# Kernel optimization log

Hardware: AMD Instinct MI355X
Metric: run time of the kernel (lower is better)

The kernel has to match this reference:

```python
import jax, jax.numpy as jnp
import numpy as np

BATCH = 4096
IN_SIZES = [1024, 1024, 1024, 1024]
EMB = 2048  # embracement_size


def setup_inputs() -> dict:
    key = jax.random.key(0)
    keys = jax.random.split(key, 3 * len(IN_SIZES))
    inp = {}
    for i, d in enumerate(IN_SIZES):
        inp[f"x{i}"] = jax.random.normal(keys[3 * i], (BATCH, d), dtype=jnp.float32)
        # Linear params (Kaiming-ish scale)
        inp[f"W{i}"] = jax.random.normal(keys[3 * i + 1], (d, EMB), dtype=jnp.float32) / np.sqrt(d)
        inp[f"b{i}"] = jax.random.normal(keys[3 * i + 2], (EMB,), dtype=jnp.float32) * 0.01
    return inp


def _sample_indices(batch, num_feats, emb):
    # availabilities=None, selection_probabilities=None -> uniform p over modalities
    # multinomial(p, num_samples=emb, replacement=True) == categorical over log p
    logits = jnp.zeros((batch, num_feats), dtype=jnp.float32)  # uniform
    k = jax.random.key(42)
    # shape (emb, batch) broadcasts against logits batch shape (batch,)
    idx = jax.random.categorical(k, logits, axis=-1, shape=(emb, batch))
    return idx.T  # [batch, emb]


def reference(x0, W0, b0, x1, W1, b1, x2, W2, b2, x3, W3, b3):
    xs = [x0, x1, x2, x3]
    Ws = [W0, W1, W2, W3]
    bs = [b0, b1, b2, b3]
    # docking: Linear + ReLU per modality -> [batch, EMB, num_feats]
    dock = jnp.stack([jax.nn.relu(x @ W + b) for x, W, b in zip(xs, Ws, bs)], axis=-1)
    B, E, F = dock.shape
    idx = _sample_indices(B, F, E)  # [B, E] int32
    # gather along modality axis (replaces one-hot multiply-sum)
    out = jnp.take_along_axis(dock, idx[:, :, None], axis=-1)[..., 0]
    return out  # [batch, EMB]
```

## Files before the change

### kernel.cpp

```cpp
#include <hip/hip_runtime.h>
#include <stdint.h>


typedef short short8 __attribute__((ext_vector_type(8)));
typedef float floatx4 __attribute__((ext_vector_type(4)));

#define B_DIM 4096
#define K_DIM 1024
#define E_DIM 2048

__device__ __forceinline__ uint32_t rotl32(uint32_t x, uint32_t r) {
  return __builtin_amdgcn_alignbit(x, x, 32u - r);
}

__device__ __forceinline__ uint16_t f2bf(float x) {
  uint32_t u = __float_as_uint(x);
  u += 0x7FFFu + ((u >> 16) & 1u);
  return (uint16_t)(u >> 16);
}

__device__ __forceinline__ void threefry(uint32_t x0, uint32_t x1,
                                         uint32_t& o0, uint32_t& o1) {
  const uint32_t ks0 = 0u;
  const uint32_t ks1 = 42u;
  const uint32_t ks2 = 0x1BD11BDAu ^ 42u;
  x0 += ks0; x1 += ks1;
#define TF_R(r) { x0 += x1; x1 = rotl32(x1, r); x1 ^= x0; }
  TF_R(13) TF_R(15) TF_R(26) TF_R(6)
  x0 += ks1; x1 += ks2 + 1u;
  TF_R(17) TF_R(29) TF_R(16) TF_R(24)
  x0 += ks2; x1 += ks0 + 2u;
  TF_R(13) TF_R(15) TF_R(26) TF_R(6)
  x0 += ks0; x1 += ks1 + 3u;
  TF_R(17) TF_R(29) TF_R(16) TF_R(24)
  x0 += ks1; x1 += ks2 + 4u;
  TF_R(13) TF_R(15) TF_R(26) TF_R(6)
  x0 += ks2; x1 += ks0 + 5u;
#undef TF_R
  o0 = x0; o1 = x1;
}

__global__ __launch_bounds__(256) void prep_kernel(
    const float* __restrict__ x0, const float* __restrict__ x1,
    const float* __restrict__ x2, const float* __restrict__ x3,
    const float* __restrict__ W0, const float* __restrict__ W1,
    const float* __restrict__ W2, const float* __restrict__ W3,
    uint16_t* __restrict__ xb, uint16_t* __restrict__ Wt,
    uint8_t* __restrict__ idx1) {
  __shared__ float tile[32][33];
  const uint32_t g = blockIdx.x;
  const int t = threadIdx.x;
  const int f = g >> 11;
  const uint32_t ip = g & 2047u;

  const float* x = (f == 0) ? x0 : (f == 1) ? x1 : (f == 2) ? x2 : x3;
  const size_t xoff = ((size_t)ip * 256 + t) * 8;
  float4 v0 = *(const float4*)(x + xoff);
  float4 v1 = *(const float4*)(x + xoff + 4);

  const float* W = (f == 0) ? W0 : (f == 1) ? W1 : (f == 2) ? W2 : W3;
  const int e0 = (int)(ip & 63) * 32, k0 = (int)(ip >> 6) * 32;
  const int tx = t & 31, ty = t >> 5;
  float wv[4];
#pragma unroll
  for (int i = 0; i < 4; ++i)
    wv[i] = W[(size_t)(k0 + ty + i * 8) * E_DIM + e0 + tx];

  const uint32_t o0i = (g * 256u + t) * 4u;
  uint32_t byte = 0;
#pragma unroll
  for (uint32_t q = 0; q < 4; ++q) {
    uint32_t c = (o0i + q) << 2;
    uint32_t best = 0, bi = 0;
#pragma unroll
    for (uint32_t ff = 0; ff < 4; ++ff) {
      uint32_t y0, y1;
      threefry(0u, c + ff, y0, y1);
      uint32_t m = (y0 ^ y1) >> 9;
      if (ff == 0) best = m;
      else if (m > best) { best = m; bi = ff; }
    }
    byte |= bi << (2 * q);
  }
  idx1[g * 256u + t] = (uint8_t)byte;

  {
    union { uint16_t h[8]; uint64_t q[2]; } p;
    p.h[0] = f2bf(v0.x); p.h[1] = f2bf(v0.y);
    p.h[2] = f2bf(v0.z); p.h[3] = f2bf(v0.w);
    p.h[4] = f2bf(v1.x); p.h[5] = f2bf(v1.y);
    p.h[6] = f2bf(v1.z); p.h[7] = f2bf(v1.w);
    uint64_t* dst = (uint64_t*)(xb + (size_t)f * B_DIM * K_DIM + xoff);
    dst[0] = p.q[0]; dst[1] = p.q[1];
  }

#pragma unroll
  for (int i = 0; i < 4; ++i) tile[ty + i * 8][tx] = wv[i];
  __syncthreads();
  {
    const int el = t >> 3, kc = (t & 7) * 4;
    union { uint16_t h[4]; uint64_t q; } p;
#pragma unroll
    for (int i = 0; i < 4; ++i) p.h[i] = f2bf(tile[kc + i][el]);
    uint16_t* dst = Wt + (size_t)f * E_DIM * K_DIM;
    *(uint64_t*)(dst + (size_t)(e0 + el) * K_DIM + k0 + kc) = p.q;
  }
}

__device__ __forceinline__ void async16(const uint16_t* g, uint16_t* lds) {
  __builtin_amdgcn_global_load_lds(
      (const __attribute__((address_space(1))) void*)g,
      (__attribute__((address_space(3))) void*)lds, 16, 0, 0);
}

#define PLANE_A ((size_t)B_DIM * K_DIM)
#define PLANE_B ((size_t)E_DIM * K_DIM)

__global__ __launch_bounds__(512, 2) void gemm_fused(
    const uint16_t* __restrict__ Ab, const uint16_t* __restrict__ Bbt,
    const uint32_t* __restrict__ idx2,
    const float* __restrict__ bias0, const float* __restrict__ bias1,
    const float* __restrict__ bias2, const float* __restrict__ bias3,
    float* __restrict__ out) {
  __shared__ uint16_t As[3][256 * 64];
  __shared__ uint16_t Bs[3][128 * 64];

  const int tid = threadIdx.x;
  const int w = tid >> 6;
  const int l = tid & 63;

  const int flat = (int)(blockIdx.y * gridDim.x + blockIdx.x);
  const int swz = (flat & 7) * 32 + (flat >> 3);
  const int mBase = (swz >> 4) * 256;
  const int nBase = (swz & 15) * 128;

  const int wm = (w >> 1) * 64;
  const int wn = (w & 1) * 64;
  const int fr = l & 15, fq = l >> 4;

  const int sr = l >> 3;
  const int sgk = ((l & 7) ^ sr) * 8;
  const uint16_t* aBase = Ab + (size_t)(mBase + 32 * w + sr) * K_DIM + sgk;
  const uint16_t* bBase = Bbt + (size_t)(nBase + 16 * w + sr) * K_DIM + sgk;

  const int b_hi0 = (mBase + wm) >> 4;
  uint32_t iw[4][4];
#pragma unroll
  for (int ni = 0; ni < 4; ++ni) {
    int col = nBase + wn + ni * 16 + fr;
#pragma unroll
    for (int mi = 0; mi < 4; ++mi)
      iw[ni][mi] = idx2[(size_t)col * (B_DIM / 16) + b_hi0 + mi];
  }
  float bz0[4], bz1[4], bz2[4], bz3[4];
#pragma unroll
  for (int ni = 0; ni < 4; ++ni) {
    int col = nBase + wn + ni * 16 + fr;
    bz0[ni] = bias0[col]; bz1[ni] = bias1[col];
    bz2[ni] = bias2[col]; bz3[ni] = bias3[col];
  }

  auto stage = [&](int t, int tb) {
    const int fA = t >> 4, ko = (t & 15) * 64;
    const uint16_t* pA = aBase + (size_t)fA * PLANE_A + ko;
    const uint16_t* pB = bBase + (size_t)fA * PLANE_B + ko;
#pragma unroll
    for (int tt = 0; tt < 4; ++tt)
      async16(pA + (size_t)(8 * tt) * K_DIM, &As[tb][(4 * w + tt) * 512]);
#pragma unroll
    for (int tt = 0; tt < 2; ++tt)
      async16(pB + (size_t)(8 * tt) * K_DIM, &Bs[tb][(2 * w + tt) * 512]);
  };

  floatx4 acc[4][4] = {};
  floatx4 res[4][4] = {};

  stage(0, 0);
  stage(1, 1);
  asm volatile("s_waitcnt vmcnt(6)" ::: "memory");
  __builtin_amdgcn_s_barrier();
  asm volatile("" ::: "memory");

  int cb = 0, tb = 2;
#pragma unroll 1
  for (int kt = 0; kt < 64; ++kt) {
    if (kt + 2 < 64) stage(kt + 2, tb);

#pragma unroll
    for (int h = 0; h < 2; ++h) {
      short8 a[4], b[4];
      const int ch = h * 4 + fq;
      const int kc = (ch ^ (fr & 7)) * 8;
#pragma unroll
      for (int mi = 0; mi < 4; ++mi)
        a[mi] = *(const short8*)&As[cb][(wm + mi * 16 + fr) * 64 + kc];
#pragma unroll
      for (int ni = 0; ni < 4; ++ni)
        b[ni] = *(const short8*)&Bs[cb][(wn + ni * 16 + fr) * 64 + kc];
      __builtin_amdgcn_s_setprio(1);
#pragma unroll
      for (int mi = 0; mi < 4; ++mi)
#pragma unroll
        for (int ni = 0; ni < 4; ++ni)
          acc[mi][ni] = __builtin_amdgcn_mfma_f32_16x16x32_bf16(
              a[mi], b[ni], acc[mi][ni], 0, 0, 0);
      __builtin_amdgcn_s_setprio(0);
    }

    if ((kt & 15) == 15) {
      const int f = kt >> 4;
#pragma unroll
      for (int ni = 0; ni < 4; ++ni) {
        float bv = (f == 0) ? bz0[ni] : (f == 1) ? bz1[ni]
                 : (f == 2) ? bz2[ni] : bz3[ni];
#pragma unroll
        for (int mi = 0; mi < 4; ++mi) {
          uint32_t wd = iw[ni][mi];
#pragma unroll
          for (int r = 0; r < 4; ++r) {
            uint32_t sel = (wd >> (2 * (fq * 4 + r))) & 3u;
            if (sel == (uint32_t)f) res[mi][ni][r] = acc[mi][ni][r] + bv;
            acc[mi][ni][r] = 0.f;
          }
        }
      }
    }

    if (kt < 62) {
      asm volatile("s_waitcnt vmcnt(6)" ::: "memory");
      __builtin_amdgcn_s_barrier();
      asm volatile("" ::: "memory");
    } else if (kt < 63) {
      asm volatile("s_waitcnt vmcnt(0)" ::: "memory");
      __builtin_amdgcn_s_barrier();
      asm volatile("" ::: "memory");
    }
    cb = (cb == 2) ? 0 : cb + 1;
    tb = (tb == 2) ? 0 : tb + 1;
  }

#pragma unroll
  for (int ni = 0; ni < 4; ++ni) {
    int col = nBase + wn + ni * 16 + fr;
#pragma unroll
    for (int mi = 0; mi < 4; ++mi) {
      int row0 = mBase + wm + mi * 16 + fq * 4;
#pragma unroll
      for (int r = 0; r < 4; ++r) {
        float o = res[mi][ni][r];
        __builtin_nontemporal_store(o > 0.f ? o : 0.f,
                                    &out[(size_t)(row0 + r) * E_DIM + col]);
      }
    }
  }
}

extern "C" void kernel_launch(void* const* d_in, const int* in_sizes, int n_in,
                              void* d_out, int out_size, void* d_ws, size_t ws_size,
                              hipStream_t stream) {
  const float* x[4]; const float* W[4]; const float* bs[4];
  for (int f = 0; f < 4; ++f) {
    x[f]  = (const float*)d_in[3 * f + 0];
    W[f]  = (const float*)d_in[3 * f + 1];
    bs[f] = (const float*)d_in[3 * f + 2];
  }
  char* ws = (char*)d_ws;
  uint16_t* xb  = (uint16_t*)ws;
  uint16_t* Wt  = (uint16_t*)(ws + (size_t)32 * 1024 * 1024);
  uint8_t*  idx1 = (uint8_t*)(ws + (size_t)48 * 1024 * 1024);
  float* out = (float*)d_out;

  prep_kernel<<<dim3(8192), dim3(256), 0, stream>>>(
      x[0], x[1], x[2], x[3], W[0], W[1], W[2], W[3], xb, Wt, idx1);
  gemm_fused<<<dim3(E_DIM / 128, B_DIM / 256), dim3(512), 0, stream>>>(
      xb, Wt, (const uint32_t*)idx1, bs[0], bs[1], bs[2], bs[3], out);
}
```

Baseline: 274.4 us.

## Shrink GEMM block tile to 128x128 with BK=32 and four-stage pipeline

The fused GEMM block tile shrinks from 256x128 with 512 threads to 128x128 with 256 threads, doubling the grid to 512 blocks. The K step is halved to 32 and the LDS ring grows from three to four buffers, so there is one more stage of prefetch, with adjusted swizzling and waitcnt thresholds. This aims to improve occupancy and load balance across CUs and to deepen latency hiding. The cost is lower operand reuse per block, more global/L2 traffic, and twice as many barriers per K.

```diff
diff --git a/kernel.cpp b/kernel.cpp
--- a/kernel.cpp
+++ b/kernel.cpp
@@ -115,33 +115,35 @@
 
 #define PLANE_A ((size_t)B_DIM * K_DIM)
 #define PLANE_B ((size_t)E_DIM * K_DIM)
-
-__global__ __launch_bounds__(512, 2) void gemm_fused(
+#define BK 32
+
+__global__ __launch_bounds__(256, 2) void gemm_fused(
     const uint16_t* __restrict__ Ab, const uint16_t* __restrict__ Bbt,
     const uint32_t* __restrict__ idx2,
     const float* __restrict__ bias0, const float* __restrict__ bias1,
     const float* __restrict__ bias2, const float* __restrict__ bias3,
     float* __restrict__ out) {
-  __shared__ uint16_t As[3][256 * 64];
-  __shared__ uint16_t Bs[3][128 * 64];
+  __shared__ uint16_t As[4][128 * BK];
+  __shared__ uint16_t Bs[4][128 * BK];
 
   const int tid = threadIdx.x;
   const int w = tid >> 6;
   const int l = tid & 63;
 
   const int flat = (int)(blockIdx.y * gridDim.x + blockIdx.x);
-  const int swz = (flat & 7) * 32 + (flat >> 3);
-  const int mBase = (swz >> 4) * 256;
+  const int swz = (flat & 7) * 64 + (flat >> 3);
+  const int mBase = (swz >> 4) * 128;
   const int nBase = (swz & 15) * 128;
 
-  const int wm = (w >> 1) * 64;
-  const int wn = (w & 1) * 64;
+  const int wm = (w >> 1) * 64, wn = (w & 1) * 64;
   const int fr = l & 15, fq = l >> 4;
 
-  const int sr = l >> 3;
-  const int sgk = ((l & 7) ^ sr) * 8;
-  const uint16_t* aBase = Ab + (size_t)(mBase + 32 * w + sr) * K_DIM + sgk;
-  const uint16_t* bBase = Bbt + (size_t)(nBase + 16 * w + sr) * K_DIM + sgk;
+  const int sRow = l >> 2;
+  const int gck = ((l & 3) ^ ((sRow >> 1) & 3)) * 8;
+  const uint16_t* aS = Ab + (size_t)(mBase + 32 * w + sRow) * K_DIM + gck;
+  const uint16_t* bS = Bbt + (size_t)(nBase + 32 * w + sRow) * K_DIM + gck;
+
+  const int kread = ((fq ^ ((fr >> 1) & 3))) * 8;
 
   const int b_hi0 = (mBase + wm) >> 4;
   uint32_t iw[4][4];
@@ -161,15 +163,13 @@
   }
 
   auto stage = [&](int t, int tb) {
-    const int fA = t >> 4, ko = (t & 15) * 64;
-    const uint16_t* pA = aBase + (size_t)fA * PLANE_A + ko;
-    const uint16_t* pB = bBase + (size_t)fA * PLANE_B + ko;
-#pragma unroll
-    for (int tt = 0; tt < 4; ++tt)
-      async16(pA + (size_t)(8 * tt) * K_DIM, &As[tb][(4 * w + tt) * 512]);
-#pragma unroll
-    for (int tt = 0; tt < 2; ++tt)
-      async16(pB + (size_t)(8 * tt) * K_DIM, &Bs[tb][(2 * w + tt) * 512]);
+    const int fA = t >> 5, ko = (t & 31) * BK;
+    const uint16_t* pA = aS + (size_t)fA * PLANE_A + ko;
+    const uint16_t* pB = bS + (size_t)fA * PLANE_B + ko;
+    async16(pA, &As[tb][(2 * w + 0) * 512]);
+    async16(pA + (size_t)16 * K_DIM, &As[tb][(2 * w + 1) * 512]);
+    async16(pB, &Bs[tb][(2 * w + 0) * 512]);
+    async16(pB + (size_t)16 * K_DIM, &Bs[tb][(2 * w + 1) * 512]);
   };
 
   floatx4 acc[4][4] = {};
@@ -177,38 +177,35 @@
 
   stage(0, 0);
   stage(1, 1);
-  asm volatile("s_waitcnt vmcnt(6)" ::: "memory");
+  stage(2, 2);
+  asm volatile("s_waitcnt vmcnt(8)" ::: "memory");
   __builtin_amdgcn_s_barrier();
   asm volatile("" ::: "memory");
 
-  int cb = 0, tb = 2;
 #pragma unroll 1
-  for (int kt = 0; kt < 64; ++kt) {
-    if (kt + 2 < 64) stage(kt + 2, tb);
-
-#pragma unroll
-    for (int h = 0; h < 2; ++h) {
-      short8 a[4], b[4];
-      const int ch = h * 4 + fq;
-      const int kc = (ch ^ (fr & 7)) * 8;
-#pragma unroll
-      for (int mi = 0; mi < 4; ++mi)
-        a[mi] = *(const short8*)&As[cb][(wm + mi * 16 + fr) * 64 + kc];
+  for (int j = 0; j < 128; ++j) {
+    if (j + 3 < 128) stage(j + 3, (j + 3) & 3);
+
+    const uint16_t* cA = &As[j & 3][0];
+    const uint16_t* cB = &Bs[j & 3][0];
+    short8 a[4], b[4];
+#pragma unroll
+    for (int mi = 0; mi < 4; ++mi)
+      a[mi] = *(const short8*)&cA[(wm + mi * 16 + fr) * BK + kread];
+#pragma unroll
+    for (int ni = 0; ni < 4; ++ni)
+      b[ni] = *(const short8*)&cB[(wn + ni * 16 + fr) * BK + kread];
+    __builtin_amdgcn_s_setprio(1);
+#pragma unroll
+    for (int mi = 0; mi < 4; ++mi)
 #pragma unroll
       for (int ni = 0; ni < 4; ++ni)
-        b[ni] = *(const short8*)&Bs[cb][(wn + ni * 16 + fr) * 64 + kc];
-      __builtin_amdgcn_s_setprio(1);
-#pragma unroll
-      for (int mi = 0; mi < 4; ++mi)
-#pragma unroll
-        for (int ni = 0; ni < 4; ++ni)
-          acc[mi][ni] = __builtin_amdgcn_mfma_f32_16x16x32_bf16(
-              a[mi], b[ni], acc[mi][ni], 0, 0, 0);
-      __builtin_amdgcn_s_setprio(0);
-    }
-
-    if ((kt & 15) == 15) {
-      const int f = kt >> 4;
+        acc[mi][ni] = __builtin_amdgcn_mfma_f32_16x16x32_bf16(
+            a[mi], b[ni], acc[mi][ni], 0, 0, 0);
+    __builtin_amdgcn_s_setprio(0);
+
+    if ((j & 31) == 31) {
+      const int f = j >> 5;
 #pragma unroll
       for (int ni = 0; ni < 4; ++ni) {
         float bv = (f == 0) ? bz0[ni] : (f == 1) ? bz1[ni]
@@ -226,17 +223,19 @@
       }
     }
 
-    if (kt < 62) {
-      asm volatile("s_waitcnt vmcnt(6)" ::: "memory");
+    if (j < 125) {
+      asm volatile("s_waitcnt vmcnt(8)" ::: "memory");
       __builtin_amdgcn_s_barrier();
       asm volatile("" ::: "memory");
-    } else if (kt < 63) {
+    } else if (j == 125) {
+      asm volatile("s_waitcnt vmcnt(4)" ::: "memory");
+      __builtin_amdgcn_s_barrier();
+      asm volatile("" ::: "memory");
+    } else if (j == 126) {
       asm volatile("s_waitcnt vmcnt(0)" ::: "memory");
       __builtin_amdgcn_s_barrier();
       asm volatile("" ::: "memory");
     }
-    cb = (cb == 2) ? 0 : cb + 1;
-    tb = (tb == 2) ? 0 : tb + 1;
   }
 
 #pragma unroll
@@ -272,6 +271,6 @@
 
   prep_kernel<<<dim3(8192), dim3(256), 0, stream>>>(
       x[0], x[1], x[2], x[3], W[0], W[1], W[2], W[3], xb, Wt, idx1);
-  gemm_fused<<<dim3(E_DIM / 128, B_DIM / 256), dim3(512), 0, stream>>>(
+  gemm_fused<<<dim3(E_DIM / 128, B_DIM / 128), dim3(256), 0, stream>>>(
       xb, Wt, (const uint32_t*)idx1, bs[0], bs[1], bs[2], bs[3], out);
 }
```

New measurement: 280.4 us. 1.02x slower.

## Split modalities across blocks with 256x256 tiles and phased ping-pong pipeline

Applied to the files above, without the earlier changes.

Changes the GEMM tiling from 256x128 tiles covering all four modalities to 256x256 tiles where each block handles two modalities (a split over the modality axis), launched as 256 blocks. Each block stores the gathered result directly at each modality fold instead of keeping a result accumulator, which works because every output element is selected from exactly one modality. The main loop becomes a double-buffered, four-phase schedule with barriers and sched_barrier that interleaves LDS reads, async global loads and MFMA bursts. The larger tiles raise register pressure (an 8x4 accumulator) and add more barriers per iteration.

```diff
diff --git a/kernel.cpp b/kernel.cpp
--- a/kernel.cpp
+++ b/kernel.cpp
@@ -116,141 +116,193 @@
 #define PLANE_A ((size_t)B_DIM * K_DIM)
 #define PLANE_B ((size_t)E_DIM * K_DIM)
 
+#define PH_IN() do { \
+    asm volatile("" ::: "memory"); \
+    __builtin_amdgcn_s_barrier(); \
+    asm volatile("s_waitcnt lgkmcnt(0)" ::: "memory"); \
+    __builtin_amdgcn_sched_barrier(0); \
+  } while (0)
+#define PH_OUT() do { \
+    asm volatile("" ::: "memory"); \
+    __builtin_amdgcn_s_barrier(); \
+    asm volatile("" ::: "memory"); \
+  } while (0)
+
 __global__ __launch_bounds__(512, 2) void gemm_fused(
     const uint16_t* __restrict__ Ab, const uint16_t* __restrict__ Bbt,
     const uint32_t* __restrict__ idx2,
     const float* __restrict__ bias0, const float* __restrict__ bias1,
     const float* __restrict__ bias2, const float* __restrict__ bias3,
     float* __restrict__ out) {
-  __shared__ uint16_t As[3][256 * 64];
-  __shared__ uint16_t Bs[3][128 * 64];
+  __shared__ uint16_t S[65536];
 
   const int tid = threadIdx.x;
+  const int l = tid & 63;
   const int w = tid >> 6;
-  const int l = tid & 63;
-
-  const int flat = (int)(blockIdx.y * gridDim.x + blockIdx.x);
+  const int wr = w >> 2, wc = w & 3;
+  const int fr = l & 15, fq = l >> 4;
+
+  const int flat = (int)blockIdx.x;
   const int swz = (flat & 7) * 32 + (flat >> 3);
-  const int mBase = (swz >> 4) * 256;
-  const int nBase = (swz & 15) * 128;
-
-  const int wm = (w >> 1) * 64;
-  const int wn = (w & 1) * 64;
-  const int fr = l & 15, fq = l >> 4;
-
-  const int sr = l >> 3;
-  const int sgk = ((l & 7) ^ sr) * 8;
-  const uint16_t* aBase = Ab + (size_t)(mBase + 32 * w + sr) * K_DIM + sgk;
-  const uint16_t* bBase = Bbt + (size_t)(nBase + 16 * w + sr) * K_DIM + sgk;
-
-  const int b_hi0 = (mBase + wm) >> 4;
-  uint32_t iw[4][4];
+  const int ks = swz >> 7;
+  const int mn = swz & 127;
+  const int mBase = (mn >> 3) * 256;
+  const int nBase = (mn & 7) * 256;
+  const int f0 = ks * 2;
+
+  const int srow = tid >> 2;
+  const int jp = (tid & 3) ^ ((tid >> 3) & 3);
+  const size_t aSrc = (size_t)(mBase + srow) * K_DIM + jp * 8;
+  const size_t bSrc = (size_t)(nBase + srow) * K_DIM + jp * 8;
+
+  auto stage = [&](int tile, int bsel, int h) {
+    if (tile >= 32) return;
+    const int buf = tile & 1;
+    const size_t po = (size_t)(f0 + (tile >> 4)) * (bsel ? PLANE_B : PLANE_A);
+    const int ko = (tile & 15) * 64 + h * 32;
+    const uint16_t* g0 = (bsel ? Bbt : Ab) + po + (bsel ? bSrc : aSrc) + ko;
+    uint16_t* d = &S[buf * 32768 + bsel * 16384 + h * 8192 + tid * 8];
+    async16(g0, d);
+    async16(g0 + (size_t)128 * K_DIM, d + 4096);
+  };
+
+  const int slot = fq ^ ((fr >> 1) & 3);
+  const int aRdB = (wr * 128 + fr) * 32 + slot * 8;
+  const int bRdB = (wc * 64 + fr) * 32 + slot * 8;
+
+  uint32_t iwp[4][2];
 #pragma unroll
   for (int ni = 0; ni < 4; ++ni) {
-    int col = nBase + wn + ni * 16 + fr;
-#pragma unroll
-    for (int mi = 0; mi < 4; ++mi)
-      iw[ni][mi] = idx2[(size_t)col * (B_DIM / 16) + b_hi0 + mi];
-  }
-  float bz0[4], bz1[4], bz2[4], bz3[4];
+    const int col = nBase + wc * 64 + ni * 16 + fr;
+#pragma unroll
+    for (int gq = 0; gq < 2; ++gq) {
+      uint32_t pk = 0;
+#pragma unroll
+      for (int q = 0; q < 4; ++q) {
+        uint32_t wd = idx2[(size_t)col * (B_DIM / 16) +
+                           ((mBase + wr * 128) >> 4) + gq * 4 + q];
+        pk |= ((wd >> (fq * 8)) & 0xFFu) << (q * 8);
+      }
+      iwp[ni][gq] = pk;
+    }
+  }
+  const float* bpl0 = (f0 == 0) ? bias0 : bias2;
+  const float* bpl1 = (f0 == 0) ? bias1 : bias3;
+  float bz[2][4];
 #pragma unroll
   for (int ni = 0; ni < 4; ++ni) {
-    int col = nBase + wn + ni * 16 + fr;
-    bz0[ni] = bias0[col]; bz1[ni] = bias1[col];
-    bz2[ni] = bias2[col]; bz3[ni] = bias3[col];
-  }
-
-  auto stage = [&](int t, int tb) {
-    const int fA = t >> 4, ko = (t & 15) * 64;
-    const uint16_t* pA = aBase + (size_t)fA * PLANE_A + ko;
-    const uint16_t* pB = bBase + (size_t)fA * PLANE_B + ko;
-#pragma unroll
-    for (int tt = 0; tt < 4; ++tt)
-      async16(pA + (size_t)(8 * tt) * K_DIM, &As[tb][(4 * w + tt) * 512]);
-#pragma unroll
-    for (int tt = 0; tt < 2; ++tt)
-      async16(pB + (size_t)(8 * tt) * K_DIM, &Bs[tb][(2 * w + tt) * 512]);
+    const int col = nBase + wc * 64 + ni * 16 + fr;
+    bz[0][ni] = bpl0[col];
+    bz[1][ni] = bpl1[col];
+  }
+
+  floatx4 acc[8][4] = {};
+
+  auto fold = [&](int pf) {
+    const uint32_t fsel = (uint32_t)(f0 + pf);
+#pragma unroll
+    for (int ni = 0; ni < 4; ++ni) {
+      const int col = nBase + wc * 64 + ni * 16 + fr;
+      const float bv = bz[pf][ni];
+#pragma unroll
+      for (int mi = 0; mi < 8; ++mi) {
+        const uint32_t byt = iwp[ni][mi >> 2] >> ((mi & 3) * 8);
+        const int row0 = mBase + wr * 128 + mi * 16 + fq * 4;
+#pragma unroll
+        for (int r = 0; r < 4; ++r) {
+          if (((byt >> (r * 2)) & 3u) == fsel) {
+            float o = acc[mi][ni][r] + bv;
+            __builtin_nontemporal_store(
+                o > 0.f ? o : 0.f, &out[(size_t)(row0 + r) * E_DIM + col]);
+          }
+          acc[mi][ni][r] = 0.f;
+        }
+      }
+    }
   };
 
-  floatx4 acc[4][4] = {};
-  floatx4 res[4][4] = {};
-
-  stage(0, 0);
-  stage(1, 1);
+  stage(0, 1, 0); stage(0, 0, 0); stage(0, 1, 1); stage(0, 0, 1);
+  stage(1, 1, 0); stage(1, 0, 0); stage(1, 1, 1);
   asm volatile("s_waitcnt vmcnt(6)" ::: "memory");
   __builtin_amdgcn_s_barrier();
   asm volatile("" ::: "memory");
 
-  int cb = 0, tb = 2;
 #pragma unroll 1
-  for (int kt = 0; kt < 64; ++kt) {
-    if (kt + 2 < 64) stage(kt + 2, tb);
-
-#pragma unroll
-    for (int h = 0; h < 2; ++h) {
-      short8 a[4], b[4];
-      const int ch = h * 4 + fq;
-      const int kc = (ch ^ (fr & 7)) * 8;
-#pragma unroll
-      for (int mi = 0; mi < 4; ++mi)
-        a[mi] = *(const short8*)&As[cb][(wm + mi * 16 + fr) * 64 + kc];
+  for (int jt = 0; jt < 32; ++jt) {
+    const uint16_t* Sa = &S[(jt & 1) * 32768 + aRdB];
+    const uint16_t* Sb = &S[(jt & 1) * 32768 + 16384 + bRdB];
+    short8 a[4], b[4];
+
+#pragma unroll
+    for (int ni = 0; ni < 4; ++ni) b[ni] = *(const short8*)&Sb[ni * 512];
+#pragma unroll
+    for (int mi = 0; mi < 4; ++mi) a[mi] = *(const short8*)&Sa[mi * 512];
+    stage(jt + 1, 0, 1);
+    PH_IN();
+    __builtin_amdgcn_s_setprio(1);
+#pragma unroll
+    for (int mi = 0; mi < 4; ++mi)
 #pragma unroll
       for (int ni = 0; ni < 4; ++ni)
-        b[ni] = *(const short8*)&Bs[cb][(wn + ni * 16 + fr) * 64 + kc];
-      __builtin_amdgcn_s_setprio(1);
-#pragma unroll
-      for (int mi = 0; mi < 4; ++mi)
-#pragma unroll
-        for (int ni = 0; ni < 4; ++ni)
-          acc[mi][ni] = __builtin_amdgcn_mfma_f32_16x16x32_bf16(
-              a[mi], b[ni], acc[mi][ni], 0, 0, 0);
-      __builtin_amdgcn_s_setprio(0);
-    }
-
-    if ((kt & 15) == 15) {
-      const int f = kt >> 4;
-#pragma unroll
-      for (int ni = 0; ni < 4; ++ni) {
-        float bv = (f == 0) ? bz0[ni] : (f == 1) ? bz1[ni]
-                 : (f == 2) ? bz2[ni] : bz3[ni];
-#pragma unroll
-        for (int mi = 0; mi < 4; ++mi) {
-          uint32_t wd = iw[ni][mi];
-#pragma unroll
-          for (int r = 0; r < 4; ++r) {
-            uint32_t sel = (wd >> (2 * (fq * 4 + r))) & 3u;
-            if (sel == (uint32_t)f) res[mi][ni][r] = acc[mi][ni][r] + bv;
-            acc[mi][ni][r] = 0.f;
-          }
-        }
-      }
-    }
-
-    if (kt < 62) {
-      asm volatile("s_waitcnt vmcnt(6)" ::: "memory");
-      __builtin_amdgcn_s_barrier();
-      asm volatile("" ::: "memory");
-    } else if (kt < 63) {
-      asm volatile("s_waitcnt vmcnt(0)" ::: "memory");
-      __builtin_amdgcn_s_barrier();
-      asm volatile("" ::: "memory");
-    }
-    cb = (cb == 2) ? 0 : cb + 1;
-    tb = (tb == 2) ? 0 : tb + 1;
-  }
-
-#pragma unroll
-  for (int ni = 0; ni < 4; ++ni) {
-    int col = nBase + wn + ni * 16 + fr;
-#pragma unroll
-    for (int mi = 0; mi < 4; ++mi) {
-      int row0 = mBase + wm + mi * 16 + fq * 4;
-#pragma unroll
-      for (int r = 0; r < 4; ++r) {
-        float o = res[mi][ni][r];
-        __builtin_nontemporal_store(o > 0.f ? o : 0.f,
-                                    &out[(size_t)(row0 + r) * E_DIM + col]);
-      }
+        acc[mi][ni] = __builtin_amdgcn_mfma_f32_16x16x32_bf16(
+            a[mi], b[ni], acc[mi][ni], 0, 0, 0);
+    __builtin_amdgcn_s_setprio(0);
+    PH_OUT();
+
+#pragma unroll
+    for (int mi = 0; mi < 4; ++mi)
+      a[mi] = *(const short8*)&Sa[(4 + mi) * 512];
+    stage(jt + 2, 1, 0);
+    PH_IN();
+    __builtin_amdgcn_s_setprio(1);
+#pragma unroll
+    for (int mi = 0; mi < 4; ++mi)
+#pragma unroll
+      for (int ni = 0; ni < 4; ++ni)
+        acc[4 + mi][ni] = __builtin_amdgcn_mfma_f32_16x16x32_bf16(
+            a[mi], b[ni], acc[4 + mi][ni], 0, 0, 0);
+    __builtin_amdgcn_s_setprio(0);
+    PH_OUT();
+
+#pragma unroll
+    for (int ni = 0; ni < 4; ++ni)
+      b[ni] = *(const short8*)&Sb[8192 + ni * 512];
+#pragma unroll
+    for (int mi = 0; mi < 4; ++mi)
+      a[mi] = *(const short8*)&Sa[8192 + mi * 512];
+    stage(jt + 2, 0, 0);
+    PH_IN();
+    __builtin_amdgcn_s_setprio(1);
+#pragma unroll
+    for (int mi = 0; mi < 4; ++mi)
+#pragma unroll
+      for (int ni = 0; ni < 4; ++ni)
+        acc[mi][ni] = __builtin_amdgcn_mfma_f32_16x16x32_bf16(
+            a[mi], b[ni], acc[mi][ni], 0, 0, 0);
+    __builtin_amdgcn_s_setprio(0);
+    PH_OUT();
+
+#pragma unroll
+    for (int mi = 0; mi < 4; ++mi)
+      a[mi] = *(const short8*)&Sa[8192 + (4 + mi) * 512];
+    stage(jt + 2, 1, 1);
+    PH_IN();
+    __builtin_amdgcn_s_setprio(1);
+#pragma unroll
+    for (int mi = 0; mi < 4; ++mi)
+#pragma unroll
+      for (int ni = 0; ni < 4; ++ni)
+        acc[4 + mi][ni] = __builtin_amdgcn_mfma_f32_16x16x32_bf16(
+            a[mi], b[ni], acc[4 + mi][ni], 0, 0, 0);
+    __builtin_amdgcn_s_setprio(0);
+
+    if (jt == 15) fold(0);
+    if (jt == 31) {
+      fold(1);
+    } else {
+      if (jt <= 29) asm volatile("s_waitcnt vmcnt(6)" ::: "memory");
+      else          asm volatile("s_waitcnt vmcnt(0)" ::: "memory");
+      PH_OUT();
     }
   }
 }
@@ -272,6 +324,6 @@
 
   prep_kernel<<<dim3(8192), dim3(256), 0, stream>>>(
       x[0], x[1], x[2], x[3], W[0], W[1], W[2], W[3], xb, Wt, idx1);
-  gemm_fused<<<dim3(E_DIM / 128, B_DIM / 256), dim3(512), 0, stream>>>(
+  gemm_fused<<<dim3(256), dim3(512), 0, stream>>>(
       xb, Wt, (const uint32_t*)idx1, bs[0], bs[1], bs[2], bs[3], out);
 }
```

Result: slower. 388.0 us (+41.4%).

## Restructure GEMM into half-step double-buffered LDS pipeline with 128x256 tiles

Applied to the files above, without the earlier changes.

The block tile changes from 256x128 to 128x256 with a 2x4 wave grid. The triple-buffered 64-wide K stages are replaced by a double buffer split into two 32-wide halves, and the next half's loads are issued between the LDS reads and the MFMAs. The goal is to hide global-to-LDS latency at finer granularity and reduce LDS footprint (96KB) while keeping the modality-select fold. It adds twice as many barriers per K-tile and a more intricate vmcnt accounting, which could introduce stalls or hazards.

```diff
diff --git a/kernel.cpp b/kernel.cpp
--- a/kernel.cpp
+++ b/kernel.cpp
@@ -116,38 +116,59 @@
 #define PLANE_A ((size_t)B_DIM * K_DIM)
 #define PLANE_B ((size_t)E_DIM * K_DIM)
 
+#define PH_IN() do { \
+    asm volatile("" ::: "memory"); \
+    __builtin_amdgcn_s_barrier(); \
+    asm volatile("s_waitcnt lgkmcnt(0)" ::: "memory"); \
+    __builtin_amdgcn_sched_barrier(0); \
+  } while (0)
+
 __global__ __launch_bounds__(512, 2) void gemm_fused(
     const uint16_t* __restrict__ Ab, const uint16_t* __restrict__ Bbt,
     const uint32_t* __restrict__ idx2,
     const float* __restrict__ bias0, const float* __restrict__ bias1,
     const float* __restrict__ bias2, const float* __restrict__ bias3,
     float* __restrict__ out) {
-  __shared__ uint16_t As[3][256 * 64];
-  __shared__ uint16_t Bs[3][128 * 64];
+  __shared__ uint16_t S[49152];
 
   const int tid = threadIdx.x;
+  const int l = tid & 63;
   const int w = tid >> 6;
-  const int l = tid & 63;
-
-  const int flat = (int)(blockIdx.y * gridDim.x + blockIdx.x);
+  const int wr = w >> 2, wc = w & 3;
+  const int fr = l & 15, fq = l >> 4;
+
+  const int flat = (int)blockIdx.x;
   const int swz = (flat & 7) * 32 + (flat >> 3);
-  const int mBase = (swz >> 4) * 256;
-  const int nBase = (swz & 15) * 128;
-
-  const int wm = (w >> 1) * 64;
-  const int wn = (w & 1) * 64;
-  const int fr = l & 15, fq = l >> 4;
-
-  const int sr = l >> 3;
-  const int sgk = ((l & 7) ^ sr) * 8;
-  const uint16_t* aBase = Ab + (size_t)(mBase + 32 * w + sr) * K_DIM + sgk;
-  const uint16_t* bBase = Bbt + (size_t)(nBase + 16 * w + sr) * K_DIM + sgk;
-
-  const int b_hi0 = (mBase + wm) >> 4;
+  const int mBase = (swz >> 3) * 128;
+  const int nBase = (swz & 7) * 256;
+
+  const int srow = tid >> 2;
+  const int jp = (tid & 3) ^ ((tid >> 3) & 3);
+  const size_t aSrc = (size_t)(mBase + srow) * K_DIM + jp * 8;
+  const size_t bSrc = (size_t)(nBase + srow) * K_DIM + jp * 8;
+
+  auto stage = [&](int t, int h) {
+    if (t >= 64) return;
+    const int f = t >> 4;
+    const int ko = (t & 15) * 64 + h * 32;
+    const int bb = (t & 1) * 24576;
+    const uint16_t* gA = Ab + (size_t)f * PLANE_A + aSrc + ko;
+    const uint16_t* gB = Bbt + (size_t)f * PLANE_B + bSrc + ko;
+    async16(gA, &S[bb + h * 4096 + tid * 8]);
+    uint16_t* dB = &S[bb + 8192 + h * 8192 + tid * 8];
+    async16(gB, dB);
+    async16(gB + (size_t)128 * K_DIM, dB + 4096);
+  };
+
+  const int slot = fq ^ ((fr >> 1) & 3);
+  const int aRd = (wr * 64 + fr) * 32 + slot * 8;
+  const int bRd = (wc * 64 + fr) * 32 + slot * 8;
+
+  const int b_hi0 = (mBase + wr * 64) >> 4;
   uint32_t iw[4][4];
 #pragma unroll
   for (int ni = 0; ni < 4; ++ni) {
-    int col = nBase + wn + ni * 16 + fr;
+    int col = nBase + wc * 64 + ni * 16 + fr;
 #pragma unroll
     for (int mi = 0; mi < 4; ++mi)
       iw[ni][mi] = idx2[(size_t)col * (B_DIM / 16) + b_hi0 + mi];
@@ -155,96 +176,104 @@
   float bz0[4], bz1[4], bz2[4], bz3[4];
 #pragma unroll
   for (int ni = 0; ni < 4; ++ni) {
-    int col = nBase + wn + ni * 16 + fr;
+    int col = nBase + wc * 64 + ni * 16 + fr;
     bz0[ni] = bias0[col]; bz1[ni] = bias1[col];
     bz2[ni] = bias2[col]; bz3[ni] = bias3[col];
   }
 
-  auto stage = [&](int t, int tb) {
-    const int fA = t >> 4, ko = (t & 15) * 64;
-    const uint16_t* pA = aBase + (size_t)fA * PLANE_A + ko;
-    const uint16_t* pB = bBase + (size_t)fA * PLANE_B + ko;
-#pragma unroll
-    for (int tt = 0; tt < 4; ++tt)
-      async16(pA + (size_t)(8 * tt) * K_DIM, &As[tb][(4 * w + tt) * 512]);
-#pragma unroll
-    for (int tt = 0; tt < 2; ++tt)
-      async16(pB + (size_t)(8 * tt) * K_DIM, &Bs[tb][(2 * w + tt) * 512]);
-  };
-
   floatx4 acc[4][4] = {};
   floatx4 res[4][4] = {};
 
+  auto fold = [&](int f) {
+#pragma unroll
+    for (int ni = 0; ni < 4; ++ni) {
+      float bv = (f == 0) ? bz0[ni] : (f == 1) ? bz1[ni]
+               : (f == 2) ? bz2[ni] : bz3[ni];
+#pragma unroll
+      for (int mi = 0; mi < 4; ++mi) {
+        uint32_t wd = iw[ni][mi];
+#pragma unroll
+        for (int r = 0; r < 4; ++r) {
+          uint32_t sel = (wd >> (2 * (fq * 4 + r))) & 3u;
+          if (sel == (uint32_t)f) res[mi][ni][r] = acc[mi][ni][r] + bv;
+          acc[mi][ni][r] = 0.f;
+        }
+      }
+    }
+  };
+
   stage(0, 0);
-  stage(1, 1);
+  stage(0, 1);
+  stage(1, 0);
   asm volatile("s_waitcnt vmcnt(6)" ::: "memory");
   __builtin_amdgcn_s_barrier();
   asm volatile("" ::: "memory");
 
-  int cb = 0, tb = 2;
 #pragma unroll 1
-  for (int kt = 0; kt < 64; ++kt) {
-    if (kt + 2 < 64) stage(kt + 2, tb);
-
-#pragma unroll
-    for (int h = 0; h < 2; ++h) {
-      short8 a[4], b[4];
-      const int ch = h * 4 + fq;
-      const int kc = (ch ^ (fr & 7)) * 8;
-#pragma unroll
-      for (int mi = 0; mi < 4; ++mi)
-        a[mi] = *(const short8*)&As[cb][(wm + mi * 16 + fr) * 64 + kc];
+  for (int jt = 0; jt < 64; ++jt) {
+    const int bb = (jt & 1) * 24576;
+    short8 a[4], b[4];
+
+#pragma unroll
+    for (int mi = 0; mi < 4; ++mi)
+      a[mi] = *(const short8*)&S[bb + aRd + mi * 512];
+#pragma unroll
+    for (int ni = 0; ni < 4; ++ni)
+      b[ni] = *(const short8*)&S[bb + 8192 + bRd + ni * 512];
+    stage(jt + 1, 1);
+    PH_IN();
+    __builtin_amdgcn_s_setprio(1);
+#pragma unroll
+    for (int mi = 0; mi < 4; ++mi)
 #pragma unroll
       for (int ni = 0; ni < 4; ++ni)
-        b[ni] = *(const short8*)&Bs[cb][(wn + ni * 16 + fr) * 64 + kc];
-      __builtin_amdgcn_s_setprio(1);
-#pragma unroll
-      for (int mi = 0; mi < 4; ++mi)
-#pragma unroll
-        for (int ni = 0; ni < 4; ++ni)
-          acc[mi][ni] = __builtin_amdgcn_mfma_f32_16x16x32_bf16(
-              a[mi], b[ni], acc[mi][ni], 0, 0, 0);
-      __builtin_amdgcn_s_setprio(0);
-    }
-
-    if ((kt & 15) == 15) {
-      const int f = kt >> 4;
-#pragma unroll
-      for (int ni = 0; ni < 4; ++ni) {
-        float bv = (f == 0) ? bz0[ni] : (f == 1) ? bz1[ni]
-                 : (f == 2) ? bz2[ni] : bz3[ni];
-#pragma unroll
-        for (int mi = 0; mi < 4; ++mi) {
-          uint32_t wd = iw[ni][mi];
-#pragma unroll
-          for (int r = 0; r < 4; ++r) {
-            uint32_t sel = (wd >> (2 * (fq * 4 + r))) & 3u;
-            if (sel == (uint32_t)f) res[mi][ni][r] = acc[mi][ni][r] + bv;
-            acc[mi][ni][r] = 0.f;
-          }
-        }
-      }
-    }
-
-    if (kt < 62) {
-      asm volatile("s_waitcnt vmcnt(6)" ::: "memory");
-      __builtin_amdgcn_s_barrier();
+        acc[mi][ni] = __builtin_amdgcn_mfma_f32_16x16x32_bf16(
+            a[mi], b[ni], acc[mi][ni], 0, 0, 0);
+    __builtin_amdgcn_s_setprio(0);
+    if (jt < 63) asm volatile("s_waitcnt vmcnt(6)" ::: "memory");
+    else         asm volatile("s_waitcnt vmcnt(0)" ::: "memory");
+    asm volatile("" ::: "memory");
+    __builtin_amdgcn_s_barrier();
+    asm volatile("" ::: "memory");
+
+#pragma unroll
+    for (int mi = 0; mi < 4; ++mi)
+      a[mi] = *(const short8*)&S[bb + 4096 + aRd + mi * 512];
+#pragma unroll
+    for (int ni = 0; ni < 4; ++ni)
+      b[ni] = *(const short8*)&S[bb + 16384 + bRd + ni * 512];
+    stage(jt + 2, 0);
+    PH_IN();
+    __builtin_amdgcn_s_setprio(1);
+#pragma unroll
+    for (int mi = 0; mi < 4; ++mi)
+#pragma unroll
+      for (int ni = 0; ni < 4; ++ni)
+        acc[mi][ni] = __builtin_amdgcn_mfma_f32_16x16x32_bf16(
+            a[mi], b[ni], acc[mi][ni], 0, 0, 0);
+    __builtin_amdgcn_s_setprio(0);
+
+    if (jt == 15) fold(0);
+    if (jt == 31) fold(1);
+    if (jt == 47) fold(2);
+
+    if (jt < 63) {
+      if (jt <= 61) asm volatile("s_waitcnt vmcnt(6)" ::: "memory");
+      else          asm volatile("s_waitcnt vmcnt(3)" ::: "memory");
       asm volatile("" ::: "memory");
-    } else if (kt < 63) {
-      asm volatile("s_waitcnt vmcnt(0)" ::: "memory");
       __builtin_amdgcn_s_barrier();
       asm volatile("" ::: "memory");
     }
-    cb = (cb == 2) ? 0 : cb + 1;
-    tb = (tb == 2) ? 0 : tb + 1;
-  }
+  }
+
+  fold(3);
 
 #pragma unroll
   for (int ni = 0; ni < 4; ++ni) {
-    int col = nBase + wn + ni * 16 + fr;
+    int col = nBase + wc * 64 + ni * 16 + fr;
 #pragma unroll
     for (int mi = 0; mi < 4; ++mi) {
-      int row0 = mBase + wm + mi * 16 + fq * 4;
+      int row0 = mBase + wr * 64 + mi * 16 + fq * 4;
 #pragma unroll
       for (int r = 0; r < 4; ++r) {
         float o = res[mi][ni][r];
@@ -272,6 +301,6 @@
 
   prep_kernel<<<dim3(8192), dim3(256), 0, stream>>>(
       x[0], x[1], x[2], x[3], W[0], W[1], W[2], W[3], xb, Wt, idx1);
-  gemm_fused<<<dim3(E_DIM / 128, B_DIM / 256), dim3(512), 0, stream>>>(
+  gemm_fused<<<dim3(256), dim3(512), 0, stream>>>(
       xb, Wt, (const uint32_t*)idx1, bs[0], bs[1], bs[2], bs[3], out);
 }
```

After: 369.8 us. 1.35x slower.
